# Kernel optimization log

Hardware: AMD Instinct MI355X
Metric: run time of the kernel (lower is better)

The kernel has to match this reference:

```python
import jax, jax.numpy as jnp
import numpy as np

N = 1_000_000          # number of RoIs
C = 4                  # num_class (foreground classes)
IMG_H, IMG_W = 1080.0, 1920.0
BBOX_MEAN = jnp.array([0.0, 0.0, 0.0, 0.0], jnp.float32)
BBOX_STD = jnp.array([0.1, 0.1, 0.2, 0.2], jnp.float32)
THR_OBJ = 0.2          # threshold_objectness
THR_CLS = 0.1          # thresholds[0]
MIN_W, MIN_H = 6.0, 6.0
MAX_CAND = 300         # nms max_candidate_n
OVERLAP = 0.5          # nms overlap_ratio
TOP_N = 100            # nms top_n


def setup_inputs() -> dict:
    key = jax.random.key(0)
    k1, k2, k3, k4, k5 = jax.random.split(key, 5)
    logits = jax.random.normal(k1, (N, C + 1), jnp.float32) * 2.0
    cls_score_softmax = jax.nn.softmax(logits, axis=-1)          # rows sum to 1, like softmax output
    bbox_pred = jax.random.normal(k2, (N, 4 * (C + 1)), jnp.float32) * 0.5
    x1 = jax.random.uniform(k3, (N,), jnp.float32, 0.0, IMG_W * 0.8)
    y1 = jax.random.uniform(k4, (N,), jnp.float32, 0.0, IMG_H * 0.8)
    wh = jax.random.uniform(k5, (N, 2), jnp.float32, 8.0, 200.0)
    rois = jnp.stack([jnp.zeros((N,), jnp.float32), x1, y1, x1 + wh[:, 0], y1 + wh[:, 1]], axis=1)
    im_info = jnp.array([IMG_H, IMG_W], jnp.float32)
    return {"cls_score_softmax": cls_score_softmax, "bbox_pred": bbox_pred, "rois": rois, "im_info": im_info}


def _pairwise_iou(b):
    # torchvision box_iou convention: area = (x2-x1)*(y2-y1), no +1
    lt = jnp.maximum(b[:, None, :2], b[None, :, :2])
    rb = jnp.minimum(b[:, None, 2:], b[None, :, 2:])
    wh = jnp.clip(rb - lt, 0.0)
    inter = wh[..., 0] * wh[..., 1]
    area = (b[:, 2] - b[:, 0]) * (b[:, 3] - b[:, 1])
    return inter / (area[:, None] + area[None, :] - inter)


def _forward(cls_score_softmax, bbox_pred, rois, im_info):
    h_img, w_img = im_info[0], im_info[1]
    # denormalize deltas and decode against rois (bbox_transform_inv_rcnn)
    deltas = (bbox_pred.reshape(-1, 4) * BBOX_STD + BBOX_MEAN).reshape(-1, C + 1, 4)
    bx = rois[:, 1:]
    w = bx[:, 2] - bx[:, 0] + 1.0
    h = bx[:, 3] - bx[:, 1] + 1.0
    cx = bx[:, 0] + 0.5 * (w - 1.0)
    cy = bx[:, 1] + 0.5 * (h - 1.0)
    pcx = deltas[:, :, 0] * w[:, None] + cx[:, None]
    pcy = deltas[:, :, 1] * h[:, None] + cy[:, None]
    pw = jnp.exp(deltas[:, :, 2]) * w[:, None]
    ph = jnp.exp(deltas[:, :, 3]) * h[:, None]
    pred = jnp.stack([pcx - 0.5 * (pw - 1.0), pcy - 0.5 * (ph - 1.0),
                      pcx + 0.5 * (pw - 1.0), pcy + 0.5 * (ph - 1.0)], axis=-1)  # [N, C+1, 4]
    # refine_out_of_map_bbox: clip to image
    pred = jnp.stack([jnp.clip(pred[..., 0], 0.0, w_img - 1.0),
                      jnp.clip(pred[..., 1], 0.0, h_img - 1.0),
                      jnp.clip(pred[..., 2], 0.0, w_img - 1.0),
                      jnp.clip(pred[..., 3], 0.0, h_img - 1.0)], axis=-1)
    # objectness + class-score filters (masked instead of compacted: jit-friendly)
    mask_obj = (1.0 - cls_score_softmax[:, 0]) >= THR_OBJ
    maxes = jnp.max(cls_score_softmax[:, 1:], axis=1)
    argmaxes = jnp.argmax(cls_score_softmax[:, 1:], axis=1) + 1
    mask_cls = maxes > THR_CLS
    # select the box of the argmax class per row
    box = jnp.take_along_axis(pred, argmaxes[:, None, None], axis=1)[:, 0, :]  # [N, 4]
    bw = box[:, 2] - box[:, 0] + 1.0
    bh = box[:, 3] - box[:, 1] + 1.0
    mask_size = (bw >= MIN_W) | (bh >= MIN_H)  # HEIGHT_OR_WIDTH
    valid = mask_obj & mask_cls & mask_size
    # top-k candidates by max class prob (invalid rows pushed below any real score)
    cand_scores = jnp.where(valid, maxes, -1.0)
    top_vals, top_idx = jax.lax.top_k(cand_scores, MAX_CAND)   # sorted descending
    cand_boxes = box[top_idx]                                   # [M, 4]
    cand_probs = cls_score_softmax[top_idx]                     # [M, C+1]
    cand_valid = top_vals > -0.5
    # greedy NMS over the (score-sorted) candidates
    iou = _pairwise_iou(cand_boxes)
    idx = jnp.arange(MAX_CAND)

    def body(i, keep):
        sup = keep[i] & (iou[i] > OVERLAP) & (idx > i)
        return keep & ~sup

    keep = jax.lax.fori_loop(0, MAX_CAND, body, cand_valid)
    # compact kept rows into the first TOP_N slots (drop-row scatter trick)
    order = jnp.cumsum(keep.astype(jnp.int32)) - 1
    slot = jnp.where(keep & (order < TOP_N), order, TOP_N)
    rows = jnp.concatenate([jnp.zeros((MAX_CAND, 1), cand_boxes.dtype), cand_boxes, cand_probs], axis=1)
    out = jnp.zeros((TOP_N + 1, rows.shape[1]), rows.dtype).at[slot].set(rows)[:TOP_N]
    return out  # [TOP_N, 1 + 4 + (C+1)] = [100, 10], zero-padded past the kept count


def reference(cls_score_softmax, bbox_pred, rois, im_info):
    return _forward(cls_score_softmax, bbox_pred, rois, im_info)
```

## Files before the change

### kernel.cpp

```cpp
#include <hip/hip_runtime.h>
#include <math.h>

#define NBINS 4096
#define CAP   4096
#define MAXC  300
#define MAXCP 320
#define TOPN  100

__device__ __forceinline__ int bin_of(float s) {
    int b = (int)(s * (float)NBINS);
    return b > NBINS-1 ? NBINS-1 : b;
}
__device__ __forceinline__ int subbin_of(float s, int tau) {
    float f = s * (float)NBINS - (float)tau;
    int sb = (int)(f * (float)NBINS);
    sb = sb < 0 ? 0 : (sb > NBINS-1 ? NBINS-1 : sb);
    return sb;
}

__device__ __forceinline__ void decode4(float x1, float y1, float x2, float y2,
                                        float4 d4, float Wimg, float Himg,
                                        float& bx1, float& by1, float& bx2, float& by2)
{
    float w  = x2 - x1 + 1.0f;
    float h  = y2 - y1 + 1.0f;
    float cx = x1 + 0.5f*(w - 1.0f);
    float cy = y1 + 0.5f*(h - 1.0f);
    float d0 = d4.x*0.1f, d1 = d4.y*0.1f, d2 = d4.z*0.2f, d3 = d4.w*0.2f;
    float pcx = d0*w + cx;
    float pcy = d1*h + cy;
    float pw  = expf(d2)*w;
    float ph  = expf(d3)*h;
    bx1 = fminf(fmaxf(pcx - 0.5f*(pw-1.0f), 0.0f), Wimg-1.0f);
    by1 = fminf(fmaxf(pcy - 0.5f*(ph-1.0f), 0.0f), Himg-1.0f);
    bx2 = fminf(fmaxf(pcx + 0.5f*(pw-1.0f), 0.0f), Wimg-1.0f);
    by2 = fminf(fmaxf(pcy + 0.5f*(ph-1.0f), 0.0f), Himg-1.0f);
}

__global__ __launch_bounds__(256)
void rcnn_pass1(const float4* __restrict__ cls4, const float4* __restrict__ bbox4,
                const float4* __restrict__ rois4, const float* __restrict__ iminfo,
                float4* __restrict__ scores4,
                unsigned int* __restrict__ hist, unsigned int* __restrict__ hist2,
                unsigned int* __restrict__ counter, int Ng)
{
    if (blockIdx.x == 0) {
        for (int k = threadIdx.x; k < NBINS; k += 256) { hist[k] = 0u; hist2[k] = 0u; }
        if (threadIdx.x == 0) *counter = 0u;
    }

    int g = blockIdx.x * blockDim.x + threadIdx.x;
    if (g >= Ng) return;

    float c[20], q[20];
    #pragma unroll
    for (int v = 0; v < 5; v++) {
        float4 cv = cls4[5*g + v];
        c[4*v] = cv.x; c[4*v+1] = cv.y; c[4*v+2] = cv.z; c[4*v+3] = cv.w;
        float4 rv = rois4[5*g + v];
        q[4*v] = rv.x; q[4*v+1] = rv.y; q[4*v+2] = rv.z; q[4*v+3] = rv.w;
    }
    float Himg = iminfo[0], Wimg = iminfo[1];

    float s[4];
    #pragma unroll
    for (int j = 0; j < 4; j++) {
        float p0 = c[5*j], p1 = c[5*j+1], p2 = c[5*j+2], p3 = c[5*j+3], p4 = c[5*j+4];
        float m = p1; int a = 1;
        if (p2 > m) { m = p2; a = 2; }
        if (p3 > m) { m = p3; a = 3; }
        if (p4 > m) { m = p4; a = 4; }
        float sc = -1.0f;
        if (((1.0f - p0) >= 0.2f) && (m > 0.1f)) {
            float4 d4 = bbox4[20*g + 5*j + a];
            float bx1, by1, bx2, by2;
            decode4(q[5*j+1], q[5*j+2], q[5*j+3], q[5*j+4], d4, Wimg, Himg, bx1, by1, bx2, by2);
            float bw = bx2 - bx1 + 1.0f;
            float bh = by2 - by1 + 1.0f;
            if ((bw >= 6.0f) || (bh >= 6.0f)) sc = m;
        }
        s[j] = sc;
    }
    scores4[g] = make_float4(s[0], s[1], s[2], s[3]);
}

__global__ __launch_bounds__(1024)
void rcnn_hist(const float4* __restrict__ scores4, unsigned int* __restrict__ hist, int Ng)
{
    __shared__ unsigned int lh[NBINS];
    const int t = threadIdx.x;
    for (int k = t; k < NBINS; k += 1024) lh[k] = 0u;
    __syncthreads();
    int stride = gridDim.x * 1024;
    for (int g = blockIdx.x * 1024 + t; g < Ng; g += stride) {
        float4 s4 = scores4[g];
        float ss[4] = { s4.x, s4.y, s4.z, s4.w };
        #pragma unroll
        for (int j = 0; j < 4; j++)
            if (ss[j] > -0.5f) atomicAdd(&lh[bin_of(ss[j])], 1u);
    }
    __syncthreads();
    for (int k = t; k < NBINS; k += 1024) {
        unsigned int v = lh[k];
        if (v) atomicAdd(&hist[k], v);
    }
}

__global__ __launch_bounds__(1024)
void rcnn_pass2(const unsigned int* __restrict__ hist, int* __restrict__ taubin)
{
    __shared__ unsigned int suf[1024];
    __shared__ int g_sh;
    int t = threadIdx.x;
    suf[t] = hist[4*t] + hist[4*t+1] + hist[4*t+2] + hist[4*t+3];
    __syncthreads();
    for (int d = 1; d < 1024; d <<= 1) {
        unsigned int add = (t + d < 1024) ? suf[t + d] : 0u;
        __syncthreads();
        suf[t] += add;
        __syncthreads();
    }
    if (t == 0) g_sh = -1;
    __syncthreads();
    if (suf[t] >= MAXC && (t == 1023 || suf[t+1] < MAXC)) g_sh = t;
    __syncthreads();
    if (t == 0) {
        int g = g_sh;
        int tau = 0;
        if (g >= 0) {
            unsigned int cum = (g == 1023) ? 0u : suf[g+1];
            tau = 4*g;
            for (int k = 3; k >= 0; k--) {
                cum += hist[4*g + k];
                if (cum >= MAXC) { tau = 4*g + k; break; }
            }
        }
        *taubin = tau;
    }
}

__global__ __launch_bounds__(1024)
void rcnn_hist2(const float4* __restrict__ scores4, const int* __restrict__ taubin,
                unsigned int* __restrict__ hist2, int Ng)
{
    __shared__ unsigned int lh[NBINS];
    const int t = threadIdx.x;
    const int tau = *taubin;
    for (int k = t; k < NBINS; k += 1024) lh[k] = 0u;
    __syncthreads();
    int stride = gridDim.x * 1024;
    for (int g = blockIdx.x * 1024 + t; g < Ng; g += stride) {
        float4 s4 = scores4[g];
        float ss[4] = { s4.x, s4.y, s4.z, s4.w };
        #pragma unroll
        for (int j = 0; j < 4; j++)
            if (ss[j] > -0.5f && bin_of(ss[j]) == tau)
                atomicAdd(&lh[subbin_of(ss[j], tau)], 1u);
    }
    __syncthreads();
    for (int k = t; k < NBINS; k += 1024) {
        unsigned int v = lh[k];
        if (v) atomicAdd(&hist2[k], v);
    }
}

__global__ __launch_bounds__(1024)
void rcnn_pass2b(const unsigned int* __restrict__ hist, const unsigned int* __restrict__ hist2,
                 const int* __restrict__ taubin, int* __restrict__ tau2out)
{
    __shared__ unsigned int red[1024];
    __shared__ unsigned int suf[1024];
    __shared__ int g_sh;
    __shared__ unsigned int need_sh;
    int t = threadIdx.x;
    int tau = *taubin;
    unsigned int acc = 0;
    for (int k = tau + 1 + t; k < NBINS; k += 1024) acc += hist[k];
    red[t] = acc;
    __syncthreads();
    for (int d = 512; d > 0; d >>= 1) { if (t < d) red[t] += red[t + d]; __syncthreads(); }
    if (t == 0) {
        unsigned int C1 = red[0];
        need_sh = (C1 >= MAXC) ? 1u : (unsigned int)(MAXC - C1);
    }
    __syncthreads();
    unsigned int need = need_sh;
    suf[t] = hist2[4*t] + hist2[4*t+1] + hist2[4*t+2] + hist2[4*t+3];
    __syncthreads();
    for (int d = 1; d < 1024; d <<= 1) {
        unsigned int add = (t + d < 1024) ? suf[t + d] : 0u;
        __syncthreads();
        suf[t] += add;
        __syncthreads();
    }
    if (t == 0) g_sh = -1;
    __syncthreads();
    if (suf[t] >= need && (t == 1023 || suf[t+1] < need)) g_sh = t;
    __syncthreads();
    if (t == 0) {
        int g = g_sh;
        int tau2 = 0;
        if (g >= 0) {
            unsigned int cum = (g == 1023) ? 0u : suf[g+1];
            tau2 = 4*g;
            for (int k = 3; k >= 0; k--) {
                cum += hist2[4*g + k];
                if (cum >= need) { tau2 = 4*g + k; break; }
            }
        }
        *tau2out = tau2;
    }
}

__global__ __launch_bounds__(256)
void rcnn_pass3(const float4* __restrict__ scores4, const int* __restrict__ taubin,
                const int* __restrict__ tau2bin,
                float* __restrict__ cscore, int* __restrict__ cidx,
                unsigned int* __restrict__ counter, int Ng)
{
    int g = blockIdx.x * blockDim.x + threadIdx.x;
    if (g >= Ng) return;
    float4 s4 = scores4[g];
    int tau = *taubin, tau2 = *tau2bin;
    float ss[4] = { s4.x, s4.y, s4.z, s4.w };
    #pragma unroll
    for (int j = 0; j < 4; j++) {
        float s = ss[j];
        if (s > -0.5f) {
            int bin = bin_of(s);
            bool sel = (bin > tau) || (bin == tau && subbin_of(s, tau) >= tau2);
            if (sel) {
                unsigned int pos = atomicAdd(counter, 1u);
                if (pos < CAP) { cscore[pos] = s; cidx[pos] = 4*g + j; }
            }
        }
    }
}

__global__ __launch_bounds__(1024)
void rcnn_final(const float* __restrict__ cls, const float* __restrict__ bbox,
                const float* __restrict__ rois, const float* __restrict__ iminfo,
                const float* __restrict__ cscore, const int* __restrict__ cidx,
                const unsigned int* __restrict__ counter, float* __restrict__ out)
{
    __shared__ float s_s[CAP];
    __shared__ int   s_id[CAP];
    __shared__ float ts[MAXC];
    __shared__ int   tid_[MAXC];
    __shared__ float bx_[MAXCP][4];
    __shared__ float pr_[MAXC][5];
    __shared__ unsigned long long sup[MAXC][5];
    __shared__ unsigned long long maskw[5];
    __shared__ float orows[TOPN*10];
    const int t  = threadIdx.x;
    const int NT = 1024;
    int M = (int)*counter; if (M > CAP) M = CAP;

    for (int i = t; i < M; i += NT)  { s_s[i] = cscore[i]; s_id[i] = cidx[i]; }
    for (int r = t; r < MAXC; r += NT) { ts[r] = -1.0f; tid_[r] = -1; }
    for (int r = t; r < MAXCP; r += NT) { bx_[r][0]=0.0f; bx_[r][1]=0.0f; bx_[r][2]=0.0f; bx_[r][3]=0.0f; }
    if (t < 5) maskw[t] = 0ull;
    for (int k = t; k < TOPN*10; k += NT) orows[k] = 0.0f;
    __syncthreads();

    for (int i = t; i < M; i += NT) {
        float si = s_s[i]; int di = s_id[i];
        int r = 0;
        for (int j = 0; j < M; j++) {
            float sj = s_s[j];
            int   dj = s_id[j];
            r += (sj > si) || (sj == si && dj < di);
        }
        if (r < MAXC) { ts[r] = si; tid_[r] = di; }
    }
    __syncthreads();

    float Himg = iminfo[0], Wimg = iminfo[1];
    for (int r = t; r < MAXC; r += NT) {
        int i = tid_[r];
        if (i >= 0) {
            float p0 = cls[5*i], p1 = cls[5*i+1], p2 = cls[5*i+2], p3 = cls[5*i+3], p4 = cls[5*i+4];
            pr_[r][0]=p0; pr_[r][1]=p1; pr_[r][2]=p2; pr_[r][3]=p3; pr_[r][4]=p4;
            float m = p1; int a = 1;
            if (p2 > m) { m = p2; a = 2; }
            if (p3 > m) { m = p3; a = 3; }
            if (p4 > m) { m = p4; a = 4; }
            float4 d4 = ((const float4*)bbox)[5*i + a];
            float bx1, by1, bx2, by2;
            decode4(rois[5*i+1], rois[5*i+2], rois[5*i+3], rois[5*i+4], d4, Wimg, Himg, bx1, by1, bx2, by2);
            bx_[r][0]=bx1; bx_[r][1]=by1; bx_[r][2]=bx2; bx_[r][3]=by2;
            atomicOr(&maskw[r>>6], 1ull << (r & 63));
        }
    }
    __syncthreads();

    for (int task = t; task < MAXC*5; task += NT) {
        int w = task / MAXC;
        int i = task - w*MAXC;
        unsigned long long bits = 0ull;
        int j0 = w << 6;
        if (j0 + 63 > i) {
            float ax1 = bx_[i][0], ay1 = bx_[i][1], ax2 = bx_[i][2], ay2 = bx_[i][3];
            float areaA = (ax2-ax1)*(ay2-ay1);
            for (int b = 0; b < 64; b++) {
                int j = j0 + b;
                float b1 = bx_[j][0], b2 = bx_[j][1], b3 = bx_[j][2], b4 = bx_[j][3];
                float lx = fmaxf(ax1, b1), ly = fmaxf(ay1, b2);
                float rx = fminf(ax2, b3), ry = fminf(ay2, b4);
                float iw = fmaxf(rx - lx, 0.0f), ih = fmaxf(ry - ly, 0.0f);
                float inter = iw * ih;
                float areaB = (b3 - b1) * (b4 - b2);
                float iou = inter / (areaA + areaB - inter);
                bits |= (iou > 0.5f) ? (1ull << b) : 0ull;
            }
            unsigned long long jgt = (i < j0) ? ~0ull
                                  : ((i - j0) >= 63 ? 0ull : ~((1ull << (i - j0 + 1)) - 1ull));
            bits &= jgt & maskw[w];
        }
        sup[i][w] = bits;
    }
    __syncthreads();

    if (t == 0) {
        unsigned long long kw[5];
        #pragma unroll
        for (int qq = 0; qq < 5; qq++) kw[qq] = maskw[qq];
        #pragma unroll
        for (int w2 = 0; w2 < 5; w2++) {
            int nb = (w2 == 4) ? (MAXC - 4*64) : 64;
            for (int b = 0; b < nb; b++) {
                int i = (w2 << 6) + b;
                unsigned long long m = ((kw[w2] >> b) & 1ull) ? ~0ull : 0ull;
                kw[0] &= ~(sup[i][0] & m);
                kw[1] &= ~(sup[i][1] & m);
                kw[2] &= ~(sup[i][2] & m);
                kw[3] &= ~(sup[i][3] & m);
                kw[4] &= ~(sup[i][4] & m);
            }
        }
        #pragma unroll
        for (int qq = 0; qq < 5; qq++) maskw[qq] = kw[qq];
    }
    __syncthreads();

    for (int r = t; r < MAXC; r += NT) {
        if ((maskw[r>>6] >> (r & 63)) & 1ull) {
            int ord = 0;
            for (int w2 = 0; w2 < (r >> 6); w2++) ord += __popcll(maskw[w2]);
            ord += __popcll(maskw[r>>6] & ((1ull << (r & 63)) - 1ull));
            if (ord < TOPN) {
                float* row = &orows[ord*10];
                row[0] = 0.0f;
                row[1] = bx_[r][0]; row[2] = bx_[r][1]; row[3] = bx_[r][2]; row[4] = bx_[r][3];
                row[5] = pr_[r][0]; row[6] = pr_[r][1]; row[7] = pr_[r][2]; row[8] = pr_[r][3]; row[9] = pr_[r][4];
            }
        }
    }
    __syncthreads();
    for (int k = t; k < TOPN*10; k += NT) out[k] = orows[k];
}

extern "C" void kernel_launch(void* const* d_in, const int* in_sizes, int n_in,
                              void* d_out, int out_size, void* d_ws, size_t ws_size,
                              hipStream_t stream)
{
    const float* cls    = (const float*)d_in[0];
    const float* bbox   = (const float*)d_in[1];
    const float* rois   = (const float*)d_in[2];
    const float* iminfo = (const float*)d_in[3];
    int N  = in_sizes[0] / 5;
    int Ng = N / 4;

    char* ws = (char*)d_ws;
    float* scores = (float*)ws;
    size_t off = ((size_t)N * 4 + 255) & ~(size_t)255;
    unsigned int* hist    = (unsigned int*)(ws + off); off += NBINS * 4;
    unsigned int* hist2   = (unsigned int*)(ws + off); off += NBINS * 4;
    int*          taubin  = (int*)(ws + off);          off += 256;
    int*          tau2bin = (int*)(ws + off);          off += 256;
    unsigned int* counter = (unsigned int*)(ws + off); off += 256;
    float*        cscore  = (float*)(ws + off);        off += CAP * 4;
    int*          cidx    = (int*)(ws + off);          off += CAP * 4;

    int blocksG = (Ng + 255) / 256;
    rcnn_pass1<<<blocksG, 256, 0, stream>>>((const float4*)cls, (const float4*)bbox,
                                            (const float4*)rois, iminfo,
                                            (float4*)scores, hist, hist2, counter, Ng);
    rcnn_hist<<<64, 1024, 0, stream>>>((const float4*)scores, hist, Ng);
    rcnn_pass2<<<1, 1024, 0, stream>>>(hist, taubin);
    rcnn_hist2<<<64, 1024, 0, stream>>>((const float4*)scores, taubin, hist2, Ng);
    rcnn_pass2b<<<1, 1024, 0, stream>>>(hist, hist2, taubin, tau2bin);
    rcnn_pass3<<<blocksG, 256, 0, stream>>>((const float4*)scores, taubin, tau2bin,
                                            cscore, cidx, counter, Ng);
    rcnn_final<<<1, 1024, 0, stream>>>(cls, bbox, rois, iminfo,
                                       cscore, cidx, counter, (float*)d_out);
}
```

Before: 226.7 us.

## Pack score/index into 64-bit sort keys and wave-parallelize greedy NMS scan

Candidates are now stored as packed 64-bit keys (score bits high, inverted index low), so the rank-by-count sort needs one integer compare per pair instead of a float compare plus tie-break. Box storage moves to float4 for vectorized LDS access. The serial single-thread greedy NMS scan becomes a 64-lane wavefront version: each lane holds suppression rows in registers and readlane broadcasts them, which removes the per-step LDS loads. The trade-offs are more register use and dependence on wave64 readlane semantics, and the packed-key ordering relies on the scores being non-negative.

Result: no change. 225.1 us (-0.7%).

```diff
diff --git a/kernel.cpp b/kernel.cpp
--- a/kernel.cpp
+++ b/kernel.cpp
@@ -16,6 +16,12 @@
     int sb = (int)(f * (float)NBINS);
     sb = sb < 0 ? 0 : (sb > NBINS-1 ? NBINS-1 : sb);
     return sb;
+}
+
+__device__ __forceinline__ unsigned long long rdlane64(unsigned long long v, int lane) {
+    unsigned int lo = (unsigned int)__builtin_amdgcn_readlane((int)(unsigned int)(v & 0xFFFFFFFFull), lane);
+    unsigned int hi = (unsigned int)__builtin_amdgcn_readlane((int)(unsigned int)(v >> 32), lane);
+    return ((unsigned long long)hi << 32) | (unsigned long long)lo;
 }
 
 __device__ __forceinline__ void decode4(float x1, float y1, float x2, float y2,
@@ -215,7 +221,7 @@
 __global__ __launch_bounds__(256)
 void rcnn_pass3(const float4* __restrict__ scores4, const int* __restrict__ taubin,
                 const int* __restrict__ tau2bin,
-                float* __restrict__ cscore, int* __restrict__ cidx,
+                unsigned long long* __restrict__ ckey,
                 unsigned int* __restrict__ counter, int Ng)
 {
     int g = blockIdx.x * blockDim.x + threadIdx.x;
@@ -231,7 +237,11 @@
             bool sel = (bin > tau) || (bin == tau && subbin_of(s, tau) >= tau2);
             if (sel) {
                 unsigned int pos = atomicAdd(counter, 1u);
-                if (pos < CAP) { cscore[pos] = s; cidx[pos] = 4*g + j; }
+                if (pos < CAP) {
+                    unsigned int idx = (unsigned int)(4*g + j);
+                    ckey[pos] = ((unsigned long long)__float_as_uint(s) << 32)
+                              | (unsigned long long)(~idx);
+                }
             }
         }
     }
@@ -240,15 +250,13 @@
 __global__ __launch_bounds__(1024)
 void rcnn_final(const float* __restrict__ cls, const float* __restrict__ bbox,
                 const float* __restrict__ rois, const float* __restrict__ iminfo,
-                const float* __restrict__ cscore, const int* __restrict__ cidx,
+                const unsigned long long* __restrict__ ckey,
                 const unsigned int* __restrict__ counter, float* __restrict__ out)
 {
-    __shared__ float s_s[CAP];
-    __shared__ int   s_id[CAP];
-    __shared__ float ts[MAXC];
-    __shared__ int   tid_[MAXC];
-    __shared__ float bx_[MAXCP][4];
-    __shared__ float pr_[MAXC][5];
+    __shared__ unsigned long long skey[CAP];
+    __shared__ int    tid_[MAXC];
+    __shared__ float4 bx4[MAXCP];
+    __shared__ float  pr_[MAXC][5];
     __shared__ unsigned long long sup[MAXC][5];
     __shared__ unsigned long long maskw[5];
     __shared__ float orows[TOPN*10];
@@ -256,22 +264,18 @@
     const int NT = 1024;
     int M = (int)*counter; if (M > CAP) M = CAP;
 
-    for (int i = t; i < M; i += NT)  { s_s[i] = cscore[i]; s_id[i] = cidx[i]; }
-    for (int r = t; r < MAXC; r += NT) { ts[r] = -1.0f; tid_[r] = -1; }
-    for (int r = t; r < MAXCP; r += NT) { bx_[r][0]=0.0f; bx_[r][1]=0.0f; bx_[r][2]=0.0f; bx_[r][3]=0.0f; }
+    for (int i = t; i < M; i += NT)  skey[i] = ckey[i];
+    for (int r = t; r < MAXC; r += NT) tid_[r] = -1;
+    for (int r = t; r < MAXCP; r += NT) bx4[r] = make_float4(0.f, 0.f, 0.f, 0.f);
     if (t < 5) maskw[t] = 0ull;
     for (int k = t; k < TOPN*10; k += NT) orows[k] = 0.0f;
     __syncthreads();
 
     for (int i = t; i < M; i += NT) {
-        float si = s_s[i]; int di = s_id[i];
+        unsigned long long ki = skey[i];
         int r = 0;
-        for (int j = 0; j < M; j++) {
-            float sj = s_s[j];
-            int   dj = s_id[j];
-            r += (sj > si) || (sj == si && dj < di);
-        }
-        if (r < MAXC) { ts[r] = si; tid_[r] = di; }
+        for (int j = 0; j < M; j++) r += (skey[j] > ki);
+        if (r < MAXC) tid_[r] = (int)(~(unsigned int)ki);
     }
     __syncthreads();
 
@@ -288,7 +292,7 @@
             float4 d4 = ((const float4*)bbox)[5*i + a];
             float bx1, by1, bx2, by2;
             decode4(rois[5*i+1], rois[5*i+2], rois[5*i+3], rois[5*i+4], d4, Wimg, Himg, bx1, by1, bx2, by2);
-            bx_[r][0]=bx1; bx_[r][1]=by1; bx_[r][2]=bx2; bx_[r][3]=by2;
+            bx4[r] = make_float4(bx1, by1, bx2, by2);
             atomicOr(&maskw[r>>6], 1ull << (r & 63));
         }
     }
@@ -300,16 +304,15 @@
         unsigned long long bits = 0ull;
         int j0 = w << 6;
         if (j0 + 63 > i) {
-            float ax1 = bx_[i][0], ay1 = bx_[i][1], ax2 = bx_[i][2], ay2 = bx_[i][3];
-            float areaA = (ax2-ax1)*(ay2-ay1);
+            float4 A = bx4[i];
+            float areaA = (A.z - A.x)*(A.w - A.y);
             for (int b = 0; b < 64; b++) {
-                int j = j0 + b;
-                float b1 = bx_[j][0], b2 = bx_[j][1], b3 = bx_[j][2], b4 = bx_[j][3];
-                float lx = fmaxf(ax1, b1), ly = fmaxf(ay1, b2);
-                float rx = fminf(ax2, b3), ry = fminf(ay2, b4);
+                float4 B = bx4[j0 + b];
+                float lx = fmaxf(A.x, B.x), ly = fmaxf(A.y, B.y);
+                float rx = fminf(A.z, B.z), ry = fminf(A.w, B.w);
                 float iw = fmaxf(rx - lx, 0.0f), ih = fmaxf(ry - ly, 0.0f);
                 float inter = iw * ih;
-                float areaB = (b3 - b1) * (b4 - b2);
+                float areaB = (B.z - B.x)*(B.w - B.y);
                 float iou = inter / (areaA + areaB - inter);
                 bits |= (iou > 0.5f) ? (1ull << b) : 0ull;
             }
@@ -321,25 +324,37 @@
     }
     __syncthreads();
 
-    if (t == 0) {
-        unsigned long long kw[5];
+    if (t < 64) {
+        unsigned long long S0[5], S1[5], S2[5], S3[5], S4[5];
         #pragma unroll
-        for (int qq = 0; qq < 5; qq++) kw[qq] = maskw[qq];
-        #pragma unroll
-        for (int w2 = 0; w2 < 5; w2++) {
-            int nb = (w2 == 4) ? (MAXC - 4*64) : 64;
-            for (int b = 0; b < nb; b++) {
-                int i = (w2 << 6) + b;
-                unsigned long long m = ((kw[w2] >> b) & 1ull) ? ~0ull : 0ull;
-                kw[0] &= ~(sup[i][0] & m);
-                kw[1] &= ~(sup[i][1] & m);
-                kw[2] &= ~(sup[i][2] & m);
-                kw[3] &= ~(sup[i][3] & m);
-                kw[4] &= ~(sup[i][4] & m);
-            }
-        }
-        #pragma unroll
-        for (int qq = 0; qq < 5; qq++) maskw[qq] = kw[qq];
+        for (int w = 0; w < 5; w++) {
+            S0[w] = sup[t][w];
+            S1[w] = sup[64 + t][w];
+            S2[w] = sup[128 + t][w];
+            S3[w] = sup[192 + t][w];
+            S4[w] = (t < MAXC - 256) ? sup[256 + t][w] : 0ull;
+        }
+        unsigned long long kw0 = maskw[0], kw1 = maskw[1], kw2 = maskw[2],
+                           kw3 = maskw[3], kw4 = maskw[4];
+#define SCAN_SET(S, kwr, COUNT)                                             \
+        for (int s2 = 0; s2 < (COUNT); s2++) {                              \
+            unsigned long long m = ((kwr >> s2) & 1ull) ? ~0ull : 0ull;     \
+            kw0 &= ~(rdlane64(S[0], s2) & m);                               \
+            kw1 &= ~(rdlane64(S[1], s2) & m);                               \
+            kw2 &= ~(rdlane64(S[2], s2) & m);                               \
+            kw3 &= ~(rdlane64(S[3], s2) & m);                               \
+            kw4 &= ~(rdlane64(S[4], s2) & m);                               \
+        }
+        SCAN_SET(S0, kw0, 64)
+        SCAN_SET(S1, kw1, 64)
+        SCAN_SET(S2, kw2, 64)
+        SCAN_SET(S3, kw3, 64)
+        SCAN_SET(S4, kw4, MAXC - 256)
+#undef SCAN_SET
+        if (t == 0) {
+            maskw[0] = kw0; maskw[1] = kw1; maskw[2] = kw2;
+            maskw[3] = kw3; maskw[4] = kw4;
+        }
     }
     __syncthreads();
 
@@ -350,9 +365,11 @@
             ord += __popcll(maskw[r>>6] & ((1ull << (r & 63)) - 1ull));
             if (ord < TOPN) {
                 float* row = &orows[ord*10];
+                float4 B = bx4[r];
                 row[0] = 0.0f;
-                row[1] = bx_[r][0]; row[2] = bx_[r][1]; row[3] = bx_[r][2]; row[4] = bx_[r][3];
-                row[5] = pr_[r][0]; row[6] = pr_[r][1]; row[7] = pr_[r][2]; row[8] = pr_[r][3]; row[9] = pr_[r][4];
+                row[1] = B.x; row[2] = B.y; row[3] = B.z; row[4] = B.w;
+                row[5] = pr_[r][0]; row[6] = pr_[r][1]; row[7] = pr_[r][2];
+                row[8] = pr_[r][3]; row[9] = pr_[r][4];
             }
         }
     }
@@ -379,8 +396,7 @@
     int*          taubin  = (int*)(ws + off);          off += 256;
     int*          tau2bin = (int*)(ws + off);          off += 256;
     unsigned int* counter = (unsigned int*)(ws + off); off += 256;
-    float*        cscore  = (float*)(ws + off);        off += CAP * 4;
-    int*          cidx    = (int*)(ws + off);          off += CAP * 4;
+    unsigned long long* ckey = (unsigned long long*)(ws + off); off += CAP * 8;
 
     int blocksG = (Ng + 255) / 256;
     rcnn_pass1<<<blocksG, 256, 0, stream>>>((const float4*)cls, (const float4*)bbox,
@@ -391,7 +407,7 @@
     rcnn_hist2<<<64, 1024, 0, stream>>>((const float4*)scores, taubin, hist2, Ng);
     rcnn_pass2b<<<1, 1024, 0, stream>>>(hist, hist2, taubin, tau2bin);
     rcnn_pass3<<<blocksG, 256, 0, stream>>>((const float4*)scores, taubin, tau2bin,
-                                            cscore, cidx, counter, Ng);
+                                            ckey, counter, Ng);
     rcnn_final<<<1, 1024, 0, stream>>>(cls, bbox, rois, iminfo,
-                                       cscore, cidx, counter, (float*)d_out);
-}
+                                       ckey, counter, (float*)d_out);
+}
```
